# Optimization experiments

Measured on AMD Instinct MI355X. Metric: run time of the kernel, lower is better.

The kernel has to match this reference:

```python
import jax, jax.numpy as jnp
import numpy as np

CTX_RADIUS = 0.02
PRED_RADIUS = 0.05

def _knn_idx(xyz, k):
    # xyz: [N,3] -> [N,k] indices of k nearest neighbors (no self-loop)
    sq = jnp.sum(xyz * xyz, axis=-1)
    d2 = sq[:, None] + sq[None, :] - 2.0 * (xyz @ xyz.T)
    n = xyz.shape[0]
    d2 = d2 + jnp.eye(n, dtype=d2.dtype) * 1e10
    return jax.lax.top_k(-d2, k)[1]

def _edgeconv(xyz, feat, k, W1, b1, W2, b2):
    # PyG EdgeConv: message = mlp([x_i, x_j - x_i]), max-aggregate over neighbors
    x = jnp.concatenate([feat, xyz], axis=-1)          # [N, C+3]
    idx = _knn_idx(xyz, k)                             # [N, k]
    xj = x[idx]                                        # [N, k, C+3]
    xi = jnp.broadcast_to(x[:, None, :], xj.shape)
    msg = jnp.concatenate([xi, xj - xi], axis=-1)      # [N, k, 2*(C+3)]
    h = jax.nn.relu(msg @ W1 + b1) @ W2 + b2           # [N, k, C]
    return jnp.max(h, axis=1)                          # [N, C]

def _offset(feat, W1, b1, W2, b2):
    return jax.nn.relu(feat @ W1 + b1) @ W2 + b2

def _unit(v):
    return v / (jnp.linalg.norm(v, axis=-1, keepdims=True) + 1e-6)

def _forward(ctx_xyz, ctx_tokens, pred_tokens, noise_ctx, noise_pred,
             Wp, bp, We1, be1, We2, be2, Wc1, bc1, Wc2, bc2,
             Wq1, bq1, Wq2, bq2, Wf1, bf1, Wf2, bf2, k):
    B, P, _ = ctx_xyz.shape
    M = pred_tokens.shape[1]
    R_CTX = noise_ctx.shape[2]
    R_PRED = noise_pred.shape[2]
    C = Wp.shape[1]
    ec = lambda xyz, feat, kk: _edgeconv(xyz, feat, kk, We1, be1, We2, be2)

    # --- context branch ---
    ctx_feat = ctx_tokens @ Wp + bp                                  # [B,P,C]
    nc = _unit(noise_ctx) * CTX_RADIUS
    xyz_ctx = (ctx_xyz[:, :, None, :] + nc).reshape(B, P * R_CTX, 3)
    feat_ctx = jnp.broadcast_to(ctx_feat[:, :, None, :], (B, P, R_CTX, C)).reshape(B, P * R_CTX, C)
    feat_ctx = jax.vmap(lambda x, f: ec(x, f, k))(xyz_ctx, feat_ctx)
    xyz_ctx = xyz_ctx + _offset(feat_ctx, Wc1, bc1, Wc2, bc2)

    # --- prediction branch (batched over B*M tiny local graphs) ---
    anchor = jnp.mean(ctx_xyz, axis=1)                               # [B,3]
    pred_feat = pred_tokens @ Wp + bp                                # [B,M,C]
    npn = _unit(noise_pred) * PRED_RADIUS
    xyz_p = (anchor[:, None, None, :] + npn).reshape(B * M, R_PRED, 3)
    feat_p = jnp.broadcast_to(pred_feat[:, :, None, :], (B, M, R_PRED, C)).reshape(B * M, R_PRED, C)
    k_pred = min(k, R_PRED - 1)
    feat_p = jax.vmap(lambda x, f: ec(x, f, k_pred))(xyz_p, feat_p)
    xyz_p = xyz_p + _offset(feat_p, Wq1, bq1, Wq2, bq2)
    xyz_p = xyz_p.reshape(B, M * R_PRED, 3)
    feat_p = feat_p.reshape(B, M * R_PRED, C)

    # --- global refinement ---
    xyz_all = jnp.concatenate([xyz_ctx, xyz_p], axis=1)
    feat_all = jnp.concatenate([feat_ctx, feat_p], axis=1)
    feat_all = jax.vmap(lambda x, f: ec(x, f, k))(xyz_all, feat_all)
    xyz_all = xyz_all + _offset(feat_all, Wf1, bf1, Wf2, bf2)
    return xyz_all

def setup_inputs():
    key = jax.random.key(0)
    ks = jax.random.split(key, 20)
    B, P, M = 4, 384, 64
    C, TOK, R_CTX, R_PRED = 128, 1024, 12, 12
    w = lambda k_, s: jax.random.normal(k_, s, jnp.float32) * 0.02
    z = lambda s: jnp.zeros(s, jnp.float32)
    return {
        "ctx_xyz": jax.random.normal(ks[0], (B, P, 3), jnp.float32),
        "ctx_tokens": jax.random.normal(ks[1], (B, P, TOK), jnp.float32),
        "pred_tokens": jax.random.normal(ks[2], (B, M, TOK), jnp.float32),
        "noise_ctx": jax.random.normal(ks[3], (B, P, R_CTX, 3), jnp.float32),
        "noise_pred": jax.random.normal(ks[4], (B, M, R_PRED, 3), jnp.float32),
        "Wp": w(ks[5], (TOK, C)), "bp": z((C,)),
        "We1": w(ks[6], (2 * (C + 3), C)), "be1": z((C,)),
        "We2": w(ks[7], (C, C)), "be2": z((C,)),
        "Wc1": w(ks[8], (C, C)), "bc1": z((C,)),
        "Wc2": w(ks[9], (C, 3)), "bc2": z((3,)),
        "Wq1": w(ks[10], (C, C)), "bq1": z((C,)),
        "Wq2": w(ks[11], (C, 3)), "bq2": z((3,)),
        "Wf1": w(ks[12], (C, C)), "bf1": z((C,)),
        "Wf2": w(ks[13], (C, 3)), "bf2": z((3,)),
        "k": 8,
    }

def reference(ctx_xyz, ctx_tokens, pred_tokens, noise_ctx, noise_pred,
              Wp, bp, We1, be1, We2, be2, Wc1, bc1, Wc2, bc2,
              Wq1, bq1, Wq2, bq2, Wf1, bf1, Wf2, bf2, k):
    return _forward(ctx_xyz, ctx_tokens, pred_tokens, noise_ctx, noise_pred,
                    Wp, bp, We1, be1, We2, be2, Wc1, bc1, Wc2, bc2,
                    Wq1, bq1, Wq2, bq2, Wf1, bf1, Wf2, bf2, k)
```

## Files before the change

kernel.cpp:

```cpp
#include <hip/hip_runtime.h>
#include <math.h>

constexpr int B_   = 4;
constexpr int P_   = 384;
constexpr int M_   = 64;
constexpr int TOK  = 1024;
constexpr int C    = 128;
constexpr int RC   = 12;
constexpr int RP   = 12;
constexpr int KNN  = 8;
constexpr int GS   = 12;
constexpr int NCTX = P_ * RC;
constexpr int NPRD = M_ * RP;
constexpr int NALL = NCTX + NPRD;
constexpr int NG1  = NCTX / GS;
constexpr int NG3  = NALL / GS;
constexpr int TROWS = B_ * P_ + B_ * M_;
constexpr int KSPLIT = 4;

constexpr int ABALL_BLOCKS = (B_ * NALL) / 8;
constexpr int KNN1_BLOCKS  = B_ * (NG1 / 4);
constexpr int KNS_BLOCKS   = (B_ * M_ * RP) / 256;
constexpr int P3G_BLOCKS   = (B_ * NALL) / 64;
constexpr int KNN3C_BLOCKS = B_ * (NG1 / 4);
constexpr int KNN3P_BLOCKS = (B_ * NPRD) / 4;

typedef __attribute__((ext_vector_type(8))) short bf16x8;
typedef __attribute__((ext_vector_type(4))) float f32x4;

__device__ inline unsigned short f32_to_bf16_rne(float x) {
  union { float f; unsigned int u; } v; v.f = x;
  unsigned int r = v.u + 0x7fffu + ((v.u >> 16) & 1u);
  return (unsigned short)(r >> 16);
}
__device__ inline float bf16_to_f32(unsigned short h) {
  union { float f; unsigned int u; } v; v.u = ((unsigned int)h) << 16;
  return v.f;
}
__device__ inline void split8(const f32x4& a0, const f32x4& a1, bf16x8& hi, bf16x8& lo) {
  float vals[8] = {a0.x, a0.y, a0.z, a0.w, a1.x, a1.y, a1.z, a1.w};
  union { unsigned short s[8]; bf16x8 v; } oh, ol;
  #pragma unroll
  for (int e = 0; e < 8; ++e) {
    unsigned short h = f32_to_bf16_rne(vals[e]);
    oh.s[e] = h;
    ol.s[e] = f32_to_bf16_rne(vals[e] - bf16_to_f32(h));
  }
  hi = oh.v; lo = ol.v;
}

__global__ __launch_bounds__(256) void prep1_kernel(const float* __restrict__ We1,
                                                    const float* __restrict__ We2,
                                                    const float* __restrict__ cxyz,
                                                    const float* __restrict__ Wc1,
                                                    const float* __restrict__ Wq1,
                                                    const float* __restrict__ Wf1,
                                                    float* __restrict__ Wcat,
                                                    unsigned short* __restrict__ we2hi,
                                                    unsigned short* __restrict__ we2lo,
                                                    float* __restrict__ anchor,
                                                    unsigned short* __restrict__ w1T_hi,
                                                    unsigned short* __restrict__ w1T_lo) {
  const int tid = threadIdx.x;
  if (blockIdx.x < 131) {
    int n = blockIdx.x * 256 + tid;
    int t = n >> 8, cc = n & 255;
    float v;
    if (cc < C) v = We1[t * C + cc] - We1[(131 + t) * C + cc];
    else        v = We1[(131 + t) * C + (cc - C)];
    Wcat[n] = v;
  } else if (blockIdx.x < 195) {
    int e = (blockIdx.x - 131) * 256 + tid;
    int n = e >> 7, k = e & 127;
    float w = We2[k * C + n];
    unsigned short h = f32_to_bf16_rne(w);
    we2hi[n * C + k] = h;
    we2lo[n * C + k] = f32_to_bf16_rne(w - bf16_to_f32(h));
  } else if (blockIdx.x == 195) {
    const int w = tid >> 6, lane = tid & 63;
    float ax = 0.f, ay = 0.f, az = 0.f;
    for (int p = lane; p < P_; p += 64) {
      const float* c = &cxyz[(w * P_ + p) * 3];
      ax += c[0]; ay += c[1]; az += c[2];
    }
    for (int o = 32; o > 0; o >>= 1) {
      ax += __shfl_down(ax, o);
      ay += __shfl_down(ay, o);
      az += __shfl_down(az, o);
    }
    if (lane == 0) {
      anchor[w * 3 + 0] = ax * (1.0f / (float)P_);
      anchor[w * 3 + 1] = ay * (1.0f / (float)P_);
      anchor[w * 3 + 2] = az * (1.0f / (float)P_);
    }
  } else {
    int e = (blockIdx.x - 196) * 256 + tid;
    int wsel = e >> 14, r = e & 16383;
    int c = r >> 7, k = r & 127;
    const float* W1s = (wsel == 0) ? Wc1 : (wsel == 1) ? Wq1 : Wf1;
    float w = W1s[k * C + c];
    unsigned short h = f32_to_bf16_rne(w);
    w1T_hi[(size_t)wsel * 16384 + c * 128 + k] = h;
    w1T_lo[(size_t)wsel * 16384 + c * 128 + k] = f32_to_bf16_rne(w - bf16_to_f32(h));
  }
}

__global__ __launch_bounds__(256) void prep2_kernel(const float* __restrict__ Wp,
                                                    const float* __restrict__ bp,
                                                    const float* __restrict__ Wcat,
                                                    const float* __restrict__ be1,
                                                    unsigned short* __restrict__ wbT_hi,
                                                    unsigned short* __restrict__ wbT_lo,
                                                    float* __restrict__ cb,
                                                    unsigned short* __restrict__ wcatT_hi,
                                                    unsigned short* __restrict__ wcatT_lo) {
  __shared__ float s_lds[4][128];
  const int tid = threadIdx.x;
  if (blockIdx.x < TOK / 4) {
    const int k0 = blockIdx.x * 4;
    for (int l = tid; l < 4 * 128; l += 256) {
      int r = l >> 7, f = l & 127;
      s_lds[r][f] = Wp[(k0 + r) * C + f];
    }
    __syncthreads();
    float acc[4] = {0.f, 0.f, 0.f, 0.f};
    #pragma unroll 4
    for (int f = 0; f < 128; ++f) {
      float wv = Wcat[f * 256 + tid];
      #pragma unroll
      for (int r = 0; r < 4; ++r) acc[r] = fmaf(s_lds[r][f], wv, acc[r]);
    }
    #pragma unroll
    for (int r = 0; r < 4; ++r) {
      unsigned short h = f32_to_bf16_rne(acc[r]);
      wbT_hi[(size_t)tid * TOK + k0 + r] = h;
      wbT_lo[(size_t)tid * TOK + k0 + r] = f32_to_bf16_rne(acc[r] - bf16_to_f32(h));
    }
  } else if (blockIdx.x == TOK / 4) {
    if (tid < 128) s_lds[0][tid] = bp[tid];
    __syncthreads();
    float a = (tid < 128) ? be1[tid] : 0.f;
    #pragma unroll 4
    for (int f = 0; f < 128; ++f) a = fmaf(s_lds[0][f], Wcat[f * 256 + tid], a);
    cb[tid] = a;
  } else {
    int e = (blockIdx.x - TOK / 4 - 1) * 256 + tid;
    int c = e >> 7, k = e & 127;
    float w = Wcat[k * 256 + c];
    unsigned short h = f32_to_bf16_rne(w);
    wcatT_hi[c * 128 + k] = h;
    wcatT_lo[c * 128 + k] = f32_to_bf16_rne(w - bf16_to_f32(h));
  }
}

__global__ __launch_bounds__(256) void build_all_kernel(const float* __restrict__ cxyz,
                                                        const float* __restrict__ noise_c,
                                                        const float* __restrict__ noise_p,
                                                        const float* __restrict__ anchor,
                                                        float* __restrict__ xyz_all,
                                                        int* __restrict__ radmax) {
  if (blockIdx.x < 72) {
    int n = blockIdx.x * 256 + threadIdx.x;
    if (n < B_ * NG3) radmax[n] = 0;
    int b = n / NCTX, i = n % NCTX, p = i / RC;
    float x = noise_c[n * 3 + 0], y = noise_c[n * 3 + 1], z = noise_c[n * 3 + 2];
    float s = 0.02f / (sqrtf(x * x + y * y + z * z) + 1e-6f);
    const float* c = &cxyz[(b * P_ + p) * 3];
    float* o = &xyz_all[(b * NALL + i) * 3];
    o[0] = c[0] + x * s;
    o[1] = c[1] + y * s;
    o[2] = c[2] + z * s;
  } else {
    int n = (blockIdx.x - 72) * 256 + threadIdx.x;
    int b = n / NPRD, i = n % NPRD;
    float x = noise_p[n * 3 + 0], y = noise_p[n * 3 + 1], z = noise_p[n * 3 + 2];
    float s = 0.05f / (sqrtf(x * x + y * y + z * z) + 1e-6f);
    const float* a = &anchor[b * 3];
    float* o = &xyz_all[(b * NALL + NCTX + i) * 3];
    o[0] = a[0] + x * s;
    o[1] = a[1] + y * s;
    o[2] = a[2] + z * s;
  }
}

__global__ __launch_bounds__(256) void t12_mfma_kernel(const float* __restrict__ ctx_tok,
                                                       const float* __restrict__ pred_tok,
                                                       const unsigned short* __restrict__ wbT_hi,
                                                       const unsigned short* __restrict__ wbT_lo,
                                                       float* __restrict__ Tpart) {
  __shared__ unsigned short ahi[64 * 128];
  __shared__ unsigned short alo[64 * 128];
  __shared__ unsigned short bhi[128 * 128];
  const int tid = threadIdx.x;
  const int r0 = blockIdx.x * 64;
  const int n0 = blockIdx.y * 128;
  const int s  = blockIdx.z;
  const float* src = (r0 < B_ * P_) ? (ctx_tok + (size_t)r0 * TOK)
                                    : (pred_tok + (size_t)(r0 - B_ * P_) * TOK);
  const int lane = tid & 63, w = tid >> 6;
  const int m = lane & 15, quad = lane >> 4;

  f32x4 acc[8];
  #pragma unroll
  for (int nt = 0; nt < 8; ++nt) acc[nt] = (f32x4){0.f, 0.f, 0.f, 0.f};

  #pragma unroll 1
  for (int kc = s * (8 / KSPLIT); kc < (s + 1) * (8 / KSPLIT); ++kc) {
    __syncthreads();
    #pragma unroll
    for (int i = 0; i < 4; ++i) {
      int task = tid + 256 * i;
      int r = task >> 4, c = task & 15;
      const float* sp = src + (size_t)r * TOK + kc * 128 + c * 8;
      f32x4 a0 = *(const f32x4*)sp;
      f32x4 a1 = *(const f32x4*)(sp + 4);
      bf16x8 oh, ol;
      split8(a0, a1, oh, ol);
      int dst = (r * 16 + (c ^ (r & 15))) * 8;
      *(bf16x8*)(ahi + dst) = oh;
      *(bf16x8*)(alo + dst) = ol;
    }
    #pragma unroll
    for (int i = 0; i < 8; ++i) {
      int task = tid + 256 * i;
      int n = task >> 4, c = task & 15;
      f32x4 v = *(const f32x4*)(wbT_hi + (size_t)(n0 + n) * TOK + kc * 128 + c * 8);
      *(f32x4*)(bhi + (n * 16 + (c ^ (n & 15))) * 8) = v;
    }
    __syncthreads();
    #pragma unroll
    for (int ks = 0; ks < 4; ++ks) {
      int c0 = ks * 4 + quad;
      int aoff = ((w * 16 + m) * 16 + (c0 ^ m)) * 8;
      bf16x8 av  = *(const bf16x8*)(ahi + aoff);
      bf16x8 av2 = *(const bf16x8*)(alo + aoff);
      #pragma unroll
      for (int nt = 0; nt < 8; ++nt) {
        int n = nt * 16 + m;
        bf16x8 bh = *(const bf16x8*)(bhi + (n * 16 + (c0 ^ m)) * 8);
        bf16x8 bl = *(const bf16x8*)(wbT_lo + (size_t)(n0 + n) * TOK + kc * 128 + c0 * 8);
        acc[nt] = __builtin_amdgcn_mfma_f32_16x16x32_bf16(av, bh, acc[nt], 0, 0, 0);
        acc[nt] = __builtin_amdgcn_mfma_f32_16x16x32_bf16(av, bl, acc[nt], 0, 0, 0);
        acc[nt] = __builtin_amdgcn_mfma_f32_16x16x32_bf16(av2, bh, acc[nt], 0, 0, 0);
      }
    }
  }
  #pragma unroll
  for (int nt = 0; nt < 8; ++nt) {
    int col = n0 + nt * 16 + m;
    #pragma unroll
    for (int reg = 0; reg < 4; ++reg) {
      int row = r0 + w * 16 + quad * 4 + reg;
      Tpart[((size_t)s * TROWS + row) * 256 + col] = acc[nt][reg];
    }
  }
}

template <int STAGE>
__device__ __forceinline__ void knn_wave_body(
    const float* __restrict__ xyz_all, const float* __restrict__ ctx_xyz,
    const float* __restrict__ anchor, const int* __restrict__ radmax,
    int b, int p, int lane,
    float4* own, int* gl, float4* tile, int* tilei,
    int* __restrict__ idx_out) {
  const int NG  = (STAGE == 1) ? NG1 : NG3;
  const float* base = xyz_all + (size_t)b * NALL * 3;
  const float* cxb  = ctx_xyz + (size_t)b * P_ * 3;
  const bool owner = lane < GS;
  const int qloc = p * GS + lane;

  auto sph = [&](int g) -> float4 {
    float4 c;
    float rad;
    if (STAGE == 1) {
      c = make_float4(cxb[g * 3 + 0], cxb[g * 3 + 1], cxb[g * 3 + 2], 0.f);
      rad = 0.0201f;
    } else {
      float moff = __int_as_float(radmax[b * NG3 + g]);
      if (g < NG1) {
        c = make_float4(cxb[g * 3 + 0], cxb[g * 3 + 1], cxb[g * 3 + 2], 0.f);
        rad = 0.0201f + moff * 1.0002f + 1e-6f;
      } else {
        c = make_float4(anchor[b * 3 + 0], anchor[b * 3 + 1], anchor[b * 3 + 2], 0.f);
        rad = 0.0501f + moff * 1.0002f + 1e-6f;
      }
    }
    c.w = rad;
    return c;
  };

  if (owner) {
    float x = base[qloc * 3 + 0], y = base[qloc * 3 + 1], z = base[qloc * 3 + 2];
    own[lane] = make_float4(x, y, z, x * x + y * y + z * z);
  }
  float qx = 0.f, qy = 0.f, qz = 0.f, sqi = 0.f;
  if (owner) {
    float4 q = own[lane];
    qx = q.x; qy = q.y; qz = q.z; sqi = q.w;
  }

  float bd[KNN];
  int   bi[KNN];
  #pragma unroll
  for (int u = 0; u < KNN; ++u) { bd[u] = 3e38f; bi[u] = 0x7fffffff; }

  #pragma unroll 1
  for (int j = 0; j < GS; ++j) {
    float4 cj = own[j];
    float d2 = sqi + cj.w - 2.0f * (qx * cj.x + qy * cj.y + qz * cj.z);
    if (owner && j != lane && d2 < bd[KNN - 1]) {
      bd[KNN - 1] = d2; bi[KNN - 1] = p * GS + j;
      #pragma unroll
      for (int u = KNN - 1; u > 0; --u) {
        if (bd[u] < bd[u - 1]) {
          float td = bd[u]; bd[u] = bd[u - 1]; bd[u - 1] = td;
          int   ti = bi[u]; bi[u] = bi[u - 1]; bi[u - 1] = ti;
        }
      }
    }
  }

  float t = owner ? bd[KNN - 1] : 0.f;
  #pragma unroll
  for (int mm = 1; mm < 64; mm <<= 1) t = fmaxf(t, __shfl_xor(t, mm));
  float r = sqrtf(fmaxf(t, 0.f)) * 1.001f + 1e-6f;

  const float4 gp = sph(p);
  const float rlim = r + gp.w;

  int ng = 0;
  #pragma unroll 1
  for (int gs0 = 0; gs0 < NG; gs0 += 64) {
    int g = gs0 + lane;
    bool ok = false;
    if (g < NG && g != p) {
      float4 gq = sph(g);
      float dx = gq.x - gp.x, dy = gq.y - gp.y, dz = gq.z - gp.z;
      float lim = rlim + gq.w;
      ok = (dx * dx + dy * dy + dz * dz) < lim * lim * 1.001f;
    }
    unsigned long long mask = __ballot(ok);
    if (ok) gl[ng + (int)__popcll(mask & ((1ull << lane) - 1ull))] = g;
    ng += (int)__popcll(mask);
  }

  const int total = ng * GS;
  #pragma unroll 1
  for (int cs = 0; cs < total; cs += 64) {
    int ci = cs + lane;
    if (ci < total) {
      int gg = gl[ci / GS];
      int j  = ci % GS;
      int jloc = gg * GS + j;
      float x = base[jloc * 3 + 0], y = base[jloc * 3 + 1], z = base[jloc * 3 + 2];
      tile[lane] = make_float4(x, y, z, x * x + y * y + z * z);
      tilei[lane] = jloc;
    }
    int nj = min(64, total - cs);
    #pragma unroll 1
    for (int jj = 0; jj < nj; ++jj) {
      float4 tt = tile[jj];
      int ti0 = tilei[jj];
      float d2 = sqi + tt.w - 2.0f * (qx * tt.x + qy * tt.y + qz * tt.z);
      if (owner && d2 < bd[KNN - 1]) {
        bd[KNN - 1] = d2; bi[KNN - 1] = ti0;
        #pragma unroll
        for (int u = KNN - 1; u > 0; --u) {
          if (bd[u] < bd[u - 1]) {
            float td = bd[u]; bd[u] = bd[u - 1]; bd[u - 1] = td;
            int   ti = bi[u]; bi[u] = bi[u - 1]; bi[u - 1] = ti;
          }
        }
      }
    }
  }

  if (owner) {
    int gid = b * NALL + qloc;
    #pragma unroll
    for (int u = 0; u < KNN; ++u) idx_out[gid * KNN + u] = b * NALL + bi[u];
  }
}

__device__ __forceinline__ void knn3_pred_wave(
    const float* __restrict__ xyz_all, const float* __restrict__ ctx_xyz,
    const float* __restrict__ anchor, const int* __restrict__ radmax,
    int b, int q, int lane, int* gl, int* __restrict__ idx_out) {
  const float* base = xyz_all + (size_t)b * NALL * 3;
  const float* cxb  = ctx_xyz + (size_t)b * P_ * 3;
  const int qloc = NCTX + q;
  const int p = NG1 + q / GS;

  const float qx = base[qloc * 3 + 0], qy = base[qloc * 3 + 1], qz = base[qloc * 3 + 2];
  const float sqi = qx * qx + qy * qy + qz * qz;

  float dcur = 3e38f;
  int   icur = 0x7fffffff;
  if (lane < GS) {
    int jloc = p * GS + lane;
    if (jloc != qloc) {
      float x = base[jloc * 3 + 0], y = base[jloc * 3 + 1], z = base[jloc * 3 + 2];
      dcur = sqi + (x * x + y * y + z * z) - 2.0f * (qx * x + qy * y + qz * z);
      icur = jloc;
    }
  }
  float t = 3e38f;
  #pragma unroll 1
  for (int r8 = 0; r8 < KNN; ++r8) {
    float d = dcur; int i = icur;
    #pragma unroll
    for (int mm = 1; mm < 64; mm <<= 1) {
      float od = __shfl_xor(d, mm);
      int   oi = __shfl_xor(i, mm);
      if (od < d || (od == d && oi < i)) { d = od; i = oi; }
    }
    t = d;
    if (icur == i) { dcur = 3e38f; icur = 0x7fffffff; }
  }
  float r = sqrtf(fmaxf(t, 0.f)) * 1.001f + 1e-6f;

  int ng = 0;
  #pragma unroll 1
  for (int gs0 = 0; gs0 < NG3; gs0 += 64) {
    int g = gs0 + lane;
    bool ok = false;
    if (g < NG3) {
      float cx, cy, cz, rad;
      float moff = __int_as_float(radmax[b * NG3 + g]) * 1.0002f + 1e-6f;
      if (g < NG1) {
        cx = cxb[g * 3 + 0]; cy = cxb[g * 3 + 1]; cz = cxb[g * 3 + 2];
        rad = 0.0201f + moff;
      } else {
        cx = anchor[b * 3 + 0]; cy = anchor[b * 3 + 1]; cz = anchor[b * 3 + 2];
        rad = 0.0501f + moff;
      }
      float dx = cx - qx, dy = cy - qy, dz = cz - qz;
      float lim = r + rad;
      ok = (dx * dx + dy * dy + dz * dz) < lim * lim * 1.001f;
    }
    unsigned long long mask = __ballot(ok);
    if (ok) gl[ng + (int)__popcll(mask & ((1ull << lane) - 1ull))] = g;
    ng += (int)__popcll(mask);
  }

  float bd[KNN];
  int   bi[KNN];
  #pragma unroll
  for (int u = 0; u < KNN; ++u) { bd[u] = 3e38f; bi[u] = 0x7fffffff; }
  const int total = ng * GS;
  #pragma unroll 2
  for (int ci = lane; ci < total; ci += 64) {
    int gg = gl[ci / GS];
    int j  = ci % GS;
    int jloc = gg * GS + j;
    float x = base[jloc * 3 + 0], y = base[jloc * 3 + 1], z = base[jloc * 3 + 2];
    float d2 = sqi + (x * x + y * y + z * z) - 2.0f * (qx * x + qy * y + qz * z);
    if (jloc != qloc && d2 < bd[KNN - 1]) {
      bd[KNN - 1] = d2; bi[KNN - 1] = jloc;
      #pragma unroll
      for (int u = KNN - 1; u > 0; --u) {
        if (bd[u] < bd[u - 1]) {
          float td = bd[u]; bd[u] = bd[u - 1]; bd[u - 1] = td;
          int   ti = bi[u]; bi[u] = bi[u - 1]; bi[u - 1] = ti;
        }
      }
    }
  }

  const int gid = b * NALL + qloc;
  #pragma unroll 1
  for (int r8 = 0; r8 < KNN; ++r8) {
    float d = bd[0]; int i = bi[0];
    #pragma unroll
    for (int mm = 1; mm < 64; mm <<= 1) {
      float od = __shfl_xor(d, mm);
      int   oi = __shfl_xor(i, mm);
      if (od < d || (od == d && oi < i)) { d = od; i = oi; }
    }
    if (lane == 0) idx_out[gid * KNN + r8] = b * NALL + i;
    if (bi[0] == i) {
      #pragma unroll
      for (int u = 0; u < KNN - 1; ++u) { bd[u] = bd[u + 1]; bi[u] = bi[u + 1]; }
      bd[KNN - 1] = 3e38f; bi[KNN - 1] = 0x7fffffff;
    }
  }
}

__global__ __launch_bounds__(256) void ab12_knn12_kernel(
    const float* __restrict__ Tp, const float* __restrict__ xyz_all,
    const float* __restrict__ Wcat, const float* __restrict__ cb,
    const float* __restrict__ ctx_xyz,
    float* __restrict__ AB, int* __restrict__ idxA) {
  __shared__ float4 own[4][GS];
  __shared__ int    gl[4][NG1];
  __shared__ float4 tile[4][64];
  __shared__ int    tilei[4][64];
  const int tid = threadIdx.x;
  if (blockIdx.x < ABALL_BLOCKS) {
    const int base = blockIdx.x * 8;
    const float wx = Wcat[128 * 256 + tid];
    const float wy = Wcat[129 * 256 + tid];
    const float wz = Wcat[130 * 256 + tid];
    const float cbv = cb[tid];
    #pragma unroll
    for (int p = 0; p < 8; ++p) {
      int n = base + p;
      int b = n / NALL, row = n % NALL;
      int trow = (row < NCTX) ? (b * (NCTX / GS) + row / GS)
                              : (B_ * P_ + b * (NPRD / GS) + (row - NCTX) / GS);
      const float* xr = xyz_all + (size_t)n * 3;
      float x = xr[0], y = xr[1], z = xr[2];
      float v = cbv;
      #pragma unroll
      for (int s = 0; s < KSPLIT; ++s)
        v += Tp[((size_t)s * TROWS + trow) * 256 + tid];
      v = fmaf(x, wx, v);
      v = fmaf(y, wy, v);
      v = fmaf(z, wz, v);
      AB[(size_t)n * 256 + tid] = v;
    }
  } else if (blockIdx.x < ABALL_BLOCKS + KNN1_BLOCKS) {
    int kblk = blockIdx.x - ABALL_BLOCKS;
    int w = tid >> 6, lane = tid & 63;
    int b = kblk / (NG1 / 4);
    int p = (kblk % (NG1 / 4)) * 4 + w;
    knn_wave_body<1>(xyz_all, ctx_xyz, nullptr, nullptr, b, p, lane,
                     own[w], gl[w], tile[w], tilei[w], idxA);
  } else {
    int q = (blockIdx.x - ABALL_BLOCKS - KNN1_BLOCKS) * 256 + tid;
    int gr = q / RP, qi = q % RP;
    int b = gr / M_, w = gr % M_;
    const float* base = xyz_all + (size_t)(b * NALL + NCTX + w * RP) * 3;
    float cx[RP], cy[RP], cz[RP], cs[RP];
    #pragma unroll
    for (int j = 0; j < RP; ++j) {
      cx[j] = base[j * 3 + 0]; cy[j] = base[j * 3 + 1]; cz[j] = base[j * 3 + 2];
      cs[j] = cx[j] * cx[j] + cy[j] * cy[j] + cz[j] * cz[j];
    }
    float qx = cx[0], qy = cy[0], qz = cz[0], sqi = cs[0];
    #pragma unroll
    for (int j = 0; j < RP; ++j) {
      if (j == qi) { qx = cx[j]; qy = cy[j]; qz = cz[j]; sqi = cs[j]; }
    }
    float bd[KNN];
    int   bi[KNN];
    #pragma unroll
    for (int u = 0; u < KNN; ++u) { bd[u] = 3e38f; bi[u] = 0; }
    #pragma unroll
    for (int j = 0; j < RP; ++j) {
      float d2 = sqi + cs[j] - 2.0f * (qx * cx[j] + qy * cy[j] + qz * cz[j]);
      if (j != qi && d2 < bd[KNN - 1]) {
        bd[KNN - 1] = d2; bi[KNN - 1] = j;
        #pragma unroll
        for (int u = KNN - 1; u > 0; --u) {
          if (bd[u] < bd[u - 1]) {
            float td = bd[u]; bd[u] = bd[u - 1]; bd[u - 1] = td;
            int   ti = bi[u]; bi[u] = bi[u - 1]; bi[u - 1] = ti;
          }
        }
      }
    }
    int gid = b * NALL + NCTX + w * RP + qi;
    #pragma unroll
    for (int u = 0; u < KNN; ++u)
      idxA[gid * KNN + u] = b * NALL + NCTX + w * RP + bi[u];
  }
}

__global__ __launch_bounds__(256) void pre3_knn3_kernel(
    const float* __restrict__ feat, const float* __restrict__ xyz_all,
    const float* __restrict__ Wcat, const float* __restrict__ be1,
    const unsigned short* __restrict__ wcatT_hi, const unsigned short* __restrict__ wcatT_lo,
    const float* __restrict__ ctx_xyz, const float* __restrict__ anchor,
    const int* __restrict__ radmax,
    float* __restrict__ AB, int* __restrict__ idx3) {
  __shared__ float4 own[4][GS];
  __shared__ int    gl[4][NG3];
  __shared__ float4 tile[4][64];
  __shared__ int    tilei[4][64];
  const int tid = threadIdx.x;
  if (blockIdx.x < P3G_BLOCKS) {
    const int lane = tid & 63, w = tid >> 6;
    const int m = lane & 15, quad = lane >> 4;
    const int r0 = blockIdx.x * 64;
    const float* arow = feat + (size_t)(r0 + w * 16 + m) * C;

    f32x4 acc[16];
    #pragma unroll
    for (int nt = 0; nt < 16; ++nt) acc[nt] = (f32x4){0.f, 0.f, 0.f, 0.f};

    #pragma unroll
    for (int ks = 0; ks < 4; ++ks) {
      int k0 = ks * 32 + quad * 8;
      f32x4 a0 = *(const f32x4*)(arow + k0);
      f32x4 a1 = *(const f32x4*)(arow + k0 + 4);
      bf16x8 ahi, alo;
      split8(a0, a1, ahi, alo);
      #pragma unroll
      for (int nt = 0; nt < 16; ++nt) {
        int n = nt * 16 + m;
        bf16x8 bh = *(const bf16x8*)(wcatT_hi + n * 128 + k0);
        bf16x8 bl = *(const bf16x8*)(wcatT_lo + n * 128 + k0);
        acc[nt] = __builtin_amdgcn_mfma_f32_16x16x32_bf16(ahi, bh, acc[nt], 0, 0, 0);
        acc[nt] = __builtin_amdgcn_mfma_f32_16x16x32_bf16(ahi, bl, acc[nt], 0, 0, 0);
        acc[nt] = __builtin_amdgcn_mfma_f32_16x16x32_bf16(alo, bh, acc[nt], 0, 0, 0);
      }
    }
    float xr[4], yr[4], zr[4];
    #pragma unroll
    for (int reg = 0; reg < 4; ++reg) {
      int row = r0 + w * 16 + quad * 4 + reg;
      xr[reg] = xyz_all[row * 3 + 0];
      yr[reg] = xyz_all[row * 3 + 1];
      zr[reg] = xyz_all[row * 3 + 2];
    }
    #pragma unroll
    for (int nt = 0; nt < 16; ++nt) {
      int col = nt * 16 + m;
      float cbv = (col < C) ? be1[col] : 0.0f;
      float wx = Wcat[128 * 256 + col];
      float wy = Wcat[129 * 256 + col];
      float wz = Wcat[130 * 256 + col];
      #pragma unroll
      for (int reg = 0; reg < 4; ++reg) {
        int row = r0 + w * 16 + quad * 4 + reg;
        float v = acc[nt][reg] + cbv;
        v = fmaf(xr[reg], wx, v);
        v = fmaf(yr[reg], wy, v);
        v = fmaf(zr[reg], wz, v);
        AB[(size_t)row * 256 + col] = v;
      }
    }
  } else if (blockIdx.x < P3G_BLOCKS + KNN3C_BLOCKS) {
    int kblk = blockIdx.x - P3G_BLOCKS;
    int w = tid >> 6, lane = tid & 63;
    int b = kblk / (NG1 / 4);
    int p = (kblk % (NG1 / 4)) * 4 + w;
    knn_wave_body<3>(xyz_all, ctx_xyz, anchor, radmax, b, p, lane,
                     own[w], gl[w], tile[w], tilei[w], idx3);
  } else {
    int kblk = blockIdx.x - P3G_BLOCKS - KNN3C_BLOCKS;
    int w = tid >> 6, lane = tid & 63;
    int wid = kblk * 4 + w;
    int b = wid / NPRD, q = wid % NPRD;
    knn3_pred_wave(xyz_all, ctx_xyz, anchor, radmax, b, q, lane, gl[w], idx3);
  }
}

__global__ __launch_bounds__(256) void conv_mfma_kernel(const float* __restrict__ AB,
                                                        const int* __restrict__ idx,
                                                        const unsigned short* __restrict__ w2hi_g,
                                                        const unsigned short* __restrict__ w2lo_g,
                                                        const float* __restrict__ be2,
                                                        float* __restrict__ feat_out) {
  __shared__ unsigned short hhi[64 * 128];
  __shared__ unsigned short hlo[64 * 128];
  __shared__ unsigned short w2hi[128 * 128];
  const int tid = threadIdx.x;
  const int base = blockIdx.x * 8;

  #pragma unroll
  for (int i = 0; i < 8; ++i) {
    int q = tid + 256 * i;
    int n = q >> 4, c = q & 15;
    f32x4 v = *(const f32x4*)(w2hi_g + n * 128 + c * 8);
    *(f32x4*)(w2hi + (n * 16 + (c ^ (n & 15))) * 8) = v;
  }

  #pragma unroll
  for (int i = 0; i < 4; ++i) {
    int task = tid + 256 * i;
    int r = task >> 4, c = task & 15;
    int p = r >> 3, nb = r & 7;
    int g = base + p;
    int j = idx[g * KNN + nb];
    const float* aP = AB + (size_t)g * 256 + c * 8;
    const float* bP = AB + (size_t)j * 256 + 128 + c * 8;
    f32x4 a0 = *(const f32x4*)aP;
    f32x4 a1 = *(const f32x4*)(aP + 4);
    f32x4 b0 = *(const f32x4*)bP;
    f32x4 b1 = *(const f32x4*)(bP + 4);
    f32x4 s0 = {fmaxf(a0.x + b0.x, 0.f), fmaxf(a0.y + b0.y, 0.f),
                fmaxf(a0.z + b0.z, 0.f), fmaxf(a0.w + b0.w, 0.f)};
    f32x4 s1 = {fmaxf(a1.x + b1.x, 0.f), fmaxf(a1.y + b1.y, 0.f),
                fmaxf(a1.z + b1.z, 0.f), fmaxf(a1.w + b1.w, 0.f)};
    bf16x8 oh, ol;
    split8(s0, s1, oh, ol);
    int dst = (r * 16 + (c ^ (r & 15))) * 8;
    *(bf16x8*)(hhi + dst) = oh;
    *(bf16x8*)(hlo + dst) = ol;
  }
  __syncthreads();

  const int lane = tid & 63, w = tid >> 6;
  const int m = lane & 15, quad = lane >> 4;
  f32x4 acc[8];
  #pragma unroll
  for (int nt = 0; nt < 8; ++nt) acc[nt] = (f32x4){0.f, 0.f, 0.f, 0.f};

  #pragma unroll 1
  for (int ks = 0; ks < 4; ++ks) {
    int c0 = ks * 4 + quad;
    int k0 = c0 * 8;
    int rowA = w * 16 + m;
    int aoff = (rowA * 16 + (c0 ^ m)) * 8;
    bf16x8 ahi = *(const bf16x8*)(hhi + aoff);
    bf16x8 alo = *(const bf16x8*)(hlo + aoff);
    #pragma unroll
    for (int nt = 0; nt < 8; ++nt) {
      int n = nt * 16 + m;
      bf16x8 bhi = *(const bf16x8*)(w2hi + (n * 16 + (c0 ^ m)) * 8);
      bf16x8 blo = *(const bf16x8*)(w2lo_g + n * 128 + k0);
      acc[nt] = __builtin_amdgcn_mfma_f32_16x16x32_bf16(ahi, bhi, acc[nt], 0, 0, 0);
      acc[nt] = __builtin_amdgcn_mfma_f32_16x16x32_bf16(ahi, blo, acc[nt], 0, 0, 0);
      acc[nt] = __builtin_amdgcn_mfma_f32_16x16x32_bf16(alo, bhi, acc[nt], 0, 0, 0);
    }
  }

  int pt = 2 * w + (quad >> 1);
  int g = base + pt;
  float* orow = feat_out + (size_t)g * C;
  bool writer = (quad & 1) == 0;
  #pragma unroll
  for (int nt = 0; nt < 8; ++nt) {
    float v = fmaxf(fmaxf(acc[nt].x, acc[nt].y), fmaxf(acc[nt].z, acc[nt].w));
    v = fmaxf(v, __shfl_xor(v, 16));
    if (writer) {
      int col = nt * 16 + m;
      orow[col] = v + be2[col];
    }
  }
}

__global__ __launch_bounds__(256) void offset_mfma_kernel(
    const float* __restrict__ feat,
    const unsigned short* __restrict__ w1T_hi_c, const unsigned short* __restrict__ w1T_lo_c,
    const float* __restrict__ b1_c, const float* __restrict__ W2_c, const float* __restrict__ b2_c,
    const unsigned short* __restrict__ w1T_hi_p, const unsigned short* __restrict__ w1T_lo_p,
    const float* __restrict__ b1_p, const float* __restrict__ W2_p, const float* __restrict__ b2_p,
    const float* __restrict__ xyz_in, float* __restrict__ xyz_out,
    int* __restrict__ radmax) {
  const int tid = threadIdx.x;
  const int lane = tid & 63, w = tid >> 6;
  const int m = lane & 15, quad = lane >> 4;
  const int r0 = blockIdx.x * 64;
  const bool isCtx = (r0 % NALL) < NCTX;

  const unsigned short* w1T_hi = isCtx ? w1T_hi_c : w1T_hi_p;
  const unsigned short* w1T_lo = isCtx ? w1T_lo_c : w1T_lo_p;
  const float* b1 = isCtx ? b1_c : b1_p;
  const float* W2 = isCtx ? W2_c : W2_p;
  const float* b2 = isCtx ? b2_c : b2_p;

  const float* arow = feat + (size_t)(r0 + w * 16 + m) * C;

  f32x4 acc[8];
  #pragma unroll
  for (int nt = 0; nt < 8; ++nt) acc[nt] = (f32x4){0.f, 0.f, 0.f, 0.f};

  #pragma unroll
  for (int ks = 0; ks < 4; ++ks) {
    int k0 = ks * 32 + quad * 8;
    f32x4 a0 = *(const f32x4*)(arow + k0);
    f32x4 a1 = *(const f32x4*)(arow + k0 + 4);
    bf16x8 ahi, alo;
    split8(a0, a1, ahi, alo);
    #pragma unroll
    for (int nt = 0; nt < 8; ++nt) {
      int n = nt * 16 + m;
      bf16x8 bh = *(const bf16x8*)(w1T_hi + n * 128 + k0);
      bf16x8 bl = *(const bf16x8*)(w1T_lo + n * 128 + k0);
      acc[nt] = __builtin_amdgcn_mfma_f32_16x16x32_bf16(ahi, bh, acc[nt], 0, 0, 0);
      acc[nt] = __builtin_amdgcn_mfma_f32_16x16x32_bf16(ahi, bl, acc[nt], 0, 0, 0);
      acc[nt] = __builtin_amdgcn_mfma_f32_16x16x32_bf16(alo, bh, acc[nt], 0, 0, 0);
    }
  }

  float p0[4] = {0.f, 0.f, 0.f, 0.f};
  float p1[4] = {0.f, 0.f, 0.f, 0.f};
  float p2[4] = {0.f, 0.f, 0.f, 0.f};
  #pragma unroll
  for (int nt = 0; nt < 8; ++nt) {
    int col = nt * 16 + m;
    float b1v = b1[col];
    float w20 = W2[col * 3 + 0], w21 = W2[col * 3 + 1], w22 = W2[col * 3 + 2];
    #pragma unroll
    for (int reg = 0; reg < 4; ++reg) {
      float h = fmaxf(acc[nt][reg] + b1v, 0.0f);
      p0[reg] = fmaf(h, w20, p0[reg]);
      p1[reg] = fmaf(h, w21, p1[reg]);
      p2[reg] = fmaf(h, w22, p2[reg]);
    }
  }
  #pragma unroll
  for (int o = 1; o < 16; o <<= 1) {
    #pragma unroll
    for (int reg = 0; reg < 4; ++reg) {
      p0[reg] += __shfl_xor(p0[reg], o);
      p1[reg] += __shfl_xor(p1[reg], o);
      p2[reg] += __shfl_xor(p2[reg], o);
    }
  }
  if (m == 0) {
    float b20 = b2[0], b21 = b2[1], b22 = b2[2];
    #pragma unroll
    for (int reg = 0; reg < 4; ++reg) {
      int nO = r0 + w * 16 + quad * 4 + reg;
      int row = nO * 3;
      float o0 = p0[reg] + b20;
      float o1 = p1[reg] + b21;
      float o2 = p2[reg] + b22;
      xyz_out[row + 0] = xyz_in[row + 0] + o0;
      xyz_out[row + 1] = xyz_in[row + 1] + o1;
      xyz_out[row + 2] = xyz_in[row + 2] + o2;
      if (radmax != nullptr) {
        int b = nO / NALL, loc = nO % NALL;
        float mag = sqrtf(o0 * o0 + o1 * o1 + o2 * o2);
        atomicMax(radmax + b * NG3 + loc / GS, __float_as_int(mag));
      }
    }
  }
}

extern "C" void kernel_launch(void* const* d_in, const int* in_sizes, int n_in,
                              void* d_out, int out_size, void* d_ws, size_t ws_size,
                              hipStream_t stream) {
  (void)in_sizes; (void)n_in; (void)out_size; (void)ws_size;
  const float* ctx_xyz   = (const float*)d_in[0];
  const float* ctx_tok   = (const float*)d_in[1];
  const float* pred_tok  = (const float*)d_in[2];
  const float* noise_ctx = (const float*)d_in[3];
  const float* noise_prd = (const float*)d_in[4];
  const float* Wp  = (const float*)d_in[5];
  const float* bp  = (const float*)d_in[6];
  const float* We1 = (const float*)d_in[7];
  const float* be1 = (const float*)d_in[8];
  const float* We2 = (const float*)d_in[9];
  const float* be2 = (const float*)d_in[10];
  const float* Wc1 = (const float*)d_in[11];
  const float* bc1 = (const float*)d_in[12];
  const float* Wc2 = (const float*)d_in[13];
  const float* bc2 = (const float*)d_in[14];
  const float* Wq1 = (const float*)d_in[15];
  const float* bq1 = (const float*)d_in[16];
  const float* Wq2 = (const float*)d_in[17];
  const float* bq2 = (const float*)d_in[18];
  const float* Wf1 = (const float*)d_in[19];
  const float* bf1 = (const float*)d_in[20];
  const float* Wf2 = (const float*)d_in[21];
  const float* bf2 = (const float*)d_in[22];
  float* out = (float*)d_out;

  float* ws        = (float*)d_ws;
  float* T         = ws;
  float* anchor    = T + TROWS * 256;
  float* xyz_all   = anchor + 16;
  float* feat_in   = xyz_all + B_ * NALL * 3;
  float* feat_out  = feat_in + B_ * NALL * C;
  float* AB        = feat_out + B_ * NALL * C;
  float* Wcat      = AB + B_ * NALL * 256;
  float* cb        = Wcat + 131 * 256;
  int*   idxA      = (int*)(cb + 256);
  int*   idx3      = idxA + B_ * NALL * KNN;
  unsigned short* we2hi = (unsigned short*)(idx3 + B_ * NALL * KNN);
  unsigned short* we2lo = we2hi + C * C;
  int*   radmax    = (int*)(we2lo + C * C);
  unsigned short* wcatT_hi = (unsigned short*)(radmax + B_ * NG3);
  unsigned short* wcatT_lo = wcatT_hi + 256 * 128;
  unsigned short* w1T_hi   = wcatT_lo + 256 * 128;
  unsigned short* w1T_lo   = w1T_hi + 3 * C * C;
  unsigned short* wbT_hi = (unsigned short*)AB;
  unsigned short* wbT_lo = wbT_hi + 256 * TOK;
  float* Tpart = feat_out;

  prep1_kernel<<<388, 256, 0, stream>>>(We1, We2, ctx_xyz, Wc1, Wq1, Wf1,
                                        Wcat, we2hi, we2lo, anchor, w1T_hi, w1T_lo);
  prep2_kernel<<<TOK / 4 + 1 + 128, 256, 0, stream>>>(Wp, bp, Wcat, be1,
                                                      wbT_hi, wbT_lo, cb,
                                                      wcatT_hi, wcatT_lo);
  build_all_kernel<<<72 + 12, 256, 0, stream>>>(ctx_xyz, noise_ctx, noise_prd, anchor,
                                                xyz_all, radmax);

  t12_mfma_kernel<<<dim3(TROWS / 64, 2, KSPLIT), 256, 0, stream>>>(ctx_tok, pred_tok,
                                                                   wbT_hi, wbT_lo, Tpart);

  ab12_knn12_kernel<<<ABALL_BLOCKS + KNN1_BLOCKS + KNS_BLOCKS, 256, 0, stream>>>(
      Tpart, xyz_all, Wcat, cb, ctx_xyz, AB, idxA);
  conv_mfma_kernel<<<ABALL_BLOCKS, 256, 0, stream>>>(AB, idxA, we2hi, we2lo, be2, feat_in);
  offset_mfma_kernel<<<(B_ * NALL) / 64, 256, 0, stream>>>(
      feat_in,
      w1T_hi, w1T_lo, bc1, Wc2, bc2,
      w1T_hi + C * C, w1T_lo + C * C, bq1, Wq2, bq2,
      xyz_all, xyz_all, radmax);

  pre3_knn3_kernel<<<P3G_BLOCKS + KNN3C_BLOCKS + KNN3P_BLOCKS, 256, 0, stream>>>(
      feat_in, xyz_all, Wcat, be1, wcatT_hi, wcatT_lo, ctx_xyz, anchor, radmax, AB, idx3);
  conv_mfma_kernel<<<ABALL_BLOCKS, 256, 0, stream>>>(AB, idx3, we2hi, we2lo, be2, feat_out);
  offset_mfma_kernel<<<(B_ * NALL) / 64, 256, 0, stream>>>(
      feat_out,
      w1T_hi + 2 * C * C, w1T_lo + 2 * C * C, bf1, Wf2, bf2,
      w1T_hi + 2 * C * C, w1T_lo + 2 * C * C, bf1, Wf2, bf2,
      xyz_all, out, nullptr);
}
```

Baseline: 375.6 us.

## Split conv A-tile staging into K halves and swizzle block order

Stages the gathered ReLU(A+B) tile into LDS in two 64-wide K halves instead of one full 128-wide tile, which halves the hhi/hlo shared buffers and should let more blocks fit per CU. Neighbor indices are preloaded into registers once and reused for both halves. Block IDs are also remapped so consecutive hardware blocks handle strided point groups, presumably to spread work across XCDs and their caches. The cost is an extra barrier pair per half and reloading AB rows in two passes.

```diff
diff --git a/kernel.cpp b/kernel.cpp
--- a/kernel.cpp
+++ b/kernel.cpp
@@ -653,11 +653,13 @@
                                                         const unsigned short* __restrict__ w2lo_g,
                                                         const float* __restrict__ be2,
                                                         float* __restrict__ feat_out) {
-  __shared__ unsigned short hhi[64 * 128];
-  __shared__ unsigned short hlo[64 * 128];
+  __shared__ unsigned short hhi[64 * 64];
+  __shared__ unsigned short hlo[64 * 64];
   __shared__ unsigned short w2hi[128 * 128];
   const int tid = threadIdx.x;
-  const int base = blockIdx.x * 8;
+  const int nb = gridDim.x;
+  const int blk = (blockIdx.x % 8) * (nb / 8) + (blockIdx.x / 8);
+  const int base = blk * 8;
 
   #pragma unroll
   for (int i = 0; i < 8; ++i) {
@@ -667,30 +669,12 @@
     *(f32x4*)(w2hi + (n * 16 + (c ^ (n & 15))) * 8) = v;
   }
 
-  #pragma unroll
-  for (int i = 0; i < 4; ++i) {
-    int task = tid + 256 * i;
-    int r = task >> 4, c = task & 15;
-    int p = r >> 3, nb = r & 7;
-    int g = base + p;
-    int j = idx[g * KNN + nb];
-    const float* aP = AB + (size_t)g * 256 + c * 8;
-    const float* bP = AB + (size_t)j * 256 + 128 + c * 8;
-    f32x4 a0 = *(const f32x4*)aP;
-    f32x4 a1 = *(const f32x4*)(aP + 4);
-    f32x4 b0 = *(const f32x4*)bP;
-    f32x4 b1 = *(const f32x4*)(bP + 4);
-    f32x4 s0 = {fmaxf(a0.x + b0.x, 0.f), fmaxf(a0.y + b0.y, 0.f),
-                fmaxf(a0.z + b0.z, 0.f), fmaxf(a0.w + b0.w, 0.f)};
-    f32x4 s1 = {fmaxf(a1.x + b1.x, 0.f), fmaxf(a1.y + b1.y, 0.f),
-                fmaxf(a1.z + b1.z, 0.f), fmaxf(a1.w + b1.w, 0.f)};
-    bf16x8 oh, ol;
-    split8(s0, s1, oh, ol);
-    int dst = (r * 16 + (c ^ (r & 15))) * 8;
-    *(bf16x8*)(hhi + dst) = oh;
-    *(bf16x8*)(hlo + dst) = ol;
-  }
-  __syncthreads();
+  int jreg[2];
+  #pragma unroll
+  for (int i = 0; i < 2; ++i) {
+    int r = (tid >> 3) + 32 * i;
+    jreg[i] = idx[(base + (r >> 3)) * KNN + (r & 7)];
+  }
 
   const int lane = tid & 63, w = tid >> 6;
   const int m = lane & 15, quad = lane >> 4;
@@ -699,21 +683,49 @@
   for (int nt = 0; nt < 8; ++nt) acc[nt] = (f32x4){0.f, 0.f, 0.f, 0.f};
 
   #pragma unroll 1
-  for (int ks = 0; ks < 4; ++ks) {
-    int c0 = ks * 4 + quad;
-    int k0 = c0 * 8;
-    int rowA = w * 16 + m;
-    int aoff = (rowA * 16 + (c0 ^ m)) * 8;
-    bf16x8 ahi = *(const bf16x8*)(hhi + aoff);
-    bf16x8 alo = *(const bf16x8*)(hlo + aoff);
-    #pragma unroll
-    for (int nt = 0; nt < 8; ++nt) {
-      int n = nt * 16 + m;
-      bf16x8 bhi = *(const bf16x8*)(w2hi + (n * 16 + (c0 ^ m)) * 8);
-      bf16x8 blo = *(const bf16x8*)(w2lo_g + n * 128 + k0);
-      acc[nt] = __builtin_amdgcn_mfma_f32_16x16x32_bf16(ahi, bhi, acc[nt], 0, 0, 0);
-      acc[nt] = __builtin_amdgcn_mfma_f32_16x16x32_bf16(ahi, blo, acc[nt], 0, 0, 0);
-      acc[nt] = __builtin_amdgcn_mfma_f32_16x16x32_bf16(alo, bhi, acc[nt], 0, 0, 0);
+  for (int kh = 0; kh < 2; ++kh) {
+    __syncthreads();
+    #pragma unroll
+    for (int i = 0; i < 2; ++i) {
+      int r = (tid >> 3) + 32 * i;
+      int c = tid & 7;
+      int g = base + (r >> 3);
+      int j = jreg[i];
+      const float* aP = AB + (size_t)g * 256 + kh * 64 + c * 8;
+      const float* bP = AB + (size_t)j * 256 + 128 + kh * 64 + c * 8;
+      f32x4 a0 = *(const f32x4*)aP;
+      f32x4 a1 = *(const f32x4*)(aP + 4);
+      f32x4 b0 = *(const f32x4*)bP;
+      f32x4 b1 = *(const f32x4*)(bP + 4);
+      f32x4 s0 = {fmaxf(a0.x + b0.x, 0.f), fmaxf(a0.y + b0.y, 0.f),
+                  fmaxf(a0.z + b0.z, 0.f), fmaxf(a0.w + b0.w, 0.f)};
+      f32x4 s1 = {fmaxf(a1.x + b1.x, 0.f), fmaxf(a1.y + b1.y, 0.f),
+                  fmaxf(a1.z + b1.z, 0.f), fmaxf(a1.w + b1.w, 0.f)};
+      bf16x8 oh, ol;
+      split8(s0, s1, oh, ol);
+      int dst = (r * 8 + (c ^ (r & 7))) * 8;
+      *(bf16x8*)(hhi + dst) = oh;
+      *(bf16x8*)(hlo + dst) = ol;
+    }
+    __syncthreads();
+    #pragma unroll
+    for (int ks2 = 0; ks2 < 2; ++ks2) {
+      int c0h = ks2 * 4 + quad;
+      int k0 = kh * 64 + c0h * 8;
+      int c16 = kh * 8 + c0h;
+      int rowA = w * 16 + m;
+      int aoff = (rowA * 8 + (c0h ^ (m & 7))) * 8;
+      bf16x8 ahi = *(const bf16x8*)(hhi + aoff);
+      bf16x8 alo = *(const bf16x8*)(hlo + aoff);
+      #pragma unroll
+      for (int nt = 0; nt < 8; ++nt) {
+        int n = nt * 16 + m;
+        bf16x8 bhi = *(const bf16x8*)(w2hi + (n * 16 + (c16 ^ m)) * 8);
+        bf16x8 blo = *(const bf16x8*)(w2lo_g + n * 128 + k0);
+        acc[nt] = __builtin_amdgcn_mfma_f32_16x16x32_bf16(ahi, bhi, acc[nt], 0, 0, 0);
+        acc[nt] = __builtin_amdgcn_mfma_f32_16x16x32_bf16(ahi, blo, acc[nt], 0, 0, 0);
+        acc[nt] = __builtin_amdgcn_mfma_f32_16x16x32_bf16(alo, bhi, acc[nt], 0, 0, 0);
+      }
     }
   }
 
```

After: 378.8 us. No clear change (+0.8%).
